# Optimization experiments

Hardware: AMD Instinct MI355X
Metric: run time of the kernel (lower is better)

The kernel has to match this reference:

```python
import jax, jax.numpy as jnp
import numpy as np

B, C, H, W = 8, 128, 128, 128
HEADS = 4
EPS_LN = 1e-6
EPS_NORM = 1e-12


def layernorm2d(x, w, b):
    # channel-wise LN over axis 1 of (B,C,H,W)
    mean = x.mean(axis=1, keepdims=True)
    var = ((x - mean) ** 2).mean(axis=1, keepdims=True)
    xn = (x - mean) / jnp.sqrt(var + EPS_LN)
    return xn * w[None, :, None, None] + b[None, :, None, None]


def conv1x1(x, w):
    # w: (O, C) pointwise conv, no bias
    return jnp.einsum('bchw,oc->bohw', x, w)


def dwconv3x3(x, w):
    # w: (C, 1, 3, 3) depthwise conv, SAME padding, no bias
    return jax.lax.conv_general_dilated(
        x, w, window_strides=(1, 1), padding='SAME',
        dimension_numbers=('NCHW', 'OIHW', 'NCHW'),
        feature_group_count=x.shape[1])


def l2norm_lastdim(x):
    n = jnp.sqrt(jnp.sum(x * x, axis=-1, keepdims=True))
    return x / jnp.maximum(n, EPS_NORM)


def setup_inputs() -> dict:
    key = jax.random.key(0)
    ks = jax.random.split(key, 12)
    s = 0.05
    return {
        'state': jax.random.normal(ks[0], (B, C, H, W), jnp.float32),
        'dark': jax.random.normal(ks[1], (B, C, H, W), jnp.float32),
        'nq_w': jnp.ones((C,), jnp.float32),
        'nq_b': jnp.zeros((C,), jnp.float32),
        'nkv_w': jnp.ones((C,), jnp.float32),
        'nkv_b': jnp.zeros((C,), jnp.float32),
        'q_pw': jax.random.normal(ks[2], (C, C), jnp.float32) * s,
        'q_dw': jax.random.normal(ks[3], (C, 1, 3, 3), jnp.float32) * s,
        'k_pw': jax.random.normal(ks[4], (C, C), jnp.float32) * s,
        'k_dw': jax.random.normal(ks[5], (C, 1, 3, 3), jnp.float32) * s,
        'v_pw': jax.random.normal(ks[6], (C, C), jnp.float32) * s,
        'v_dw': jax.random.normal(ks[7], (C, 1, 3, 3), jnp.float32) * s,
        'proj_w': jax.random.normal(ks[8], (C, C), jnp.float32) * s,
        'temperature': jnp.ones((HEADS, 1, 1), jnp.float32),
    }


def reference(state, dark, nq_w, nq_b, nkv_w, nkv_b, q_pw, q_dw, k_pw, k_dw,
              v_pw, v_dw, proj_w, temperature):
    b, c, h, w = state.shape
    dc = c // HEADS
    residual = state

    q = dwconv3x3(conv1x1(layernorm2d(state, nq_w, nq_b), q_pw), q_dw)
    k = dwconv3x3(conv1x1(layernorm2d(dark, nkv_w, nkv_b), k_pw), k_dw)
    v = dwconv3x3(conv1x1(dark, v_pw), v_dw)

    q = q.reshape(b, HEADS, dc, h * w)
    k = k.reshape(b, HEADS, dc, h * w)
    v = v.reshape(b, HEADS, dc, h * w)

    q = l2norm_lastdim(q)
    k = l2norm_lastdim(k)

    # channel-wise attention map: (b, heads, dc, dc)
    attn = jnp.einsum('bhcd,bhed->bhce', q, k) * temperature[None]
    attn = jax.nn.softmax(attn, axis=-1)

    out = jnp.einsum('bhce,bhed->bhcd', attn, v).reshape(b, c, h, w)
    return conv1x1(out, proj_w) + residual
```

## Files before the change

kernel.cpp:

```cpp
#include <hip/hip_runtime.h>
#include <hip/hip_bf16.h>
#include <cstdint>

#define BB 8
#define CC 128
#define HH 128
#define WWID 128
#define HW (HH * WWID)
#define NHEADS 4
#define DC (CC / NHEADS)

typedef unsigned short u16x8 __attribute__((ext_vector_type(8)));
typedef unsigned short u16x4 __attribute__((ext_vector_type(4)));
typedef short s16x8 __attribute__((ext_vector_type(8)));
typedef float f32x4 __attribute__((ext_vector_type(4)));

__device__ __forceinline__ float bf2f(unsigned short u) {
  union { unsigned int i; float f; } c;
  c.i = ((unsigned int)u) << 16;
  return c.f;
}
__device__ __forceinline__ unsigned short f2bf(float f) {
  __hip_bfloat16 h = __float2bfloat16(f);
  return *reinterpret_cast<unsigned short*>(&h);
}

__device__ __forceinline__ void quad_transpose(float& v0, float& v1, float& v2,
                                               float& v3, int r) {
  float u0 = __shfl_xor(v0, 1), u1 = __shfl_xor(v1, 1);
  float u2 = __shfl_xor(v2, 1), u3 = __shfl_xor(v3, 1);
  if ((r & 1) == 0) { v1 = u0; v3 = u2; } else { v0 = u1; v2 = u3; }
  u0 = __shfl_xor(v0, 2); u1 = __shfl_xor(v1, 2);
  u2 = __shfl_xor(v2, 2); u3 = __shfl_xor(v3, 2);
  if ((r & 2) == 0) { v2 = u0; v3 = u1; } else { v0 = u2; v1 = u3; }
}

__global__ __launch_bounds__(128) void prep_weights_kernel(
    const float* __restrict__ q_pw, const float* __restrict__ k_pw,
    const float* __restrict__ v_pw, const float* __restrict__ proj_w,
    const float* __restrict__ nq_w, const float* __restrict__ nq_b,
    const float* __restrict__ nkv_w, const float* __restrict__ nkv_b,
    unsigned short* __restrict__ Wq, unsigned short* __restrict__ Wkv,
    unsigned short* __restrict__ Wproj, float* __restrict__ S1q,
    float* __restrict__ S2q, float* __restrict__ S1k, float* __restrict__ S2k) {
  int o = threadIdx.x;
  int which = blockIdx.x;
  if (which == 0) {
    float s1 = 0.f, s2 = 0.f;
    for (int c = 0; c < CC; ++c) {
      float w = q_pw[o * CC + c];
      float wl = w * nq_w[c];
      s1 += wl;
      s2 += w * nq_b[c];
      Wq[o * CC + c] = f2bf(wl);
    }
    S1q[o] = s1;
    S2q[o] = s2;
  } else if (which == 1) {
    float s1 = 0.f, s2 = 0.f;
    for (int c = 0; c < CC; ++c) {
      float w = k_pw[o * CC + c];
      float wl = w * nkv_w[c];
      s1 += wl;
      s2 += w * nkv_b[c];
      Wkv[o * CC + c] = f2bf(wl);
    }
    S1k[o] = s1;
    S2k[o] = s2;
  } else if (which == 2) {
    for (int c = 0; c < CC; ++c) Wkv[(128 + o) * CC + c] = f2bf(v_pw[o * CC + c]);
  } else {
    for (int c = 0; c < CC; ++c) Wproj[o * CC + c] = f2bf(proj_w[o * CC + c]);
  }
}

template <int MT, int LN_ROWS, int IN_BF16, int OUT_F32, int DO_RES>
__global__ __launch_bounds__(256) void conv_mfma_kernel(
    const void* __restrict__ Xv, const unsigned short* __restrict__ Wbf,
    const float* __restrict__ S1, const float* __restrict__ S2,
    const float* __restrict__ res, unsigned short* __restrict__ Out0,
    unsigned short* __restrict__ Out1, float* __restrict__ OutF) {
  constexpr int MPW = MT / 4;
  __shared__ unsigned short Xs[64 * 128];
  __shared__ float sstat[2][4][64];
  __shared__ float muA[64], rrA[64];

  int tid = threadIdx.x;
  int lane = tid & 63, wid = tid >> 6;
  int b = blockIdx.y;
  int p0 = blockIdx.x * 64;

  int r = tid & 3;
  int pg = (tid >> 2) & 15;
  float s = 0.f, ss = 0.f;
  size_t xbase = (size_t)b * CC * HW + p0 + pg * 4;
#pragma unroll
  for (int i = 0; i < 8; ++i) {
    int cb = i * 16 + wid * 4;
    int ch = cb + r;
    float v0, v1, v2, v3;
    if (IN_BF16) {
      u16x4 u = *(const u16x4*)((const unsigned short*)Xv + xbase + (size_t)ch * HW);
      v0 = bf2f(u[0]); v1 = bf2f(u[1]); v2 = bf2f(u[2]); v3 = bf2f(u[3]);
    } else {
      float4 f = *(const float4*)((const float*)Xv + xbase + (size_t)ch * HW);
      v0 = f.x; v1 = f.y; v2 = f.z; v3 = f.w;
    }
    quad_transpose(v0, v1, v2, v3, r);
    if (LN_ROWS > 0) {
      s += v0 + v1 + v2 + v3;
      ss += v0 * v0 + v1 * v1 + v2 * v2 + v3 * v3;
    }
    int p = pg * 4 + r;
    u16x4 o;
    o[0] = f2bf(v0); o[1] = f2bf(v1); o[2] = f2bf(v2); o[3] = f2bf(v3);
    *(u16x4*)((char*)Xs + p * 256 + ((cb * 2) ^ ((p & 7) << 4))) = o;
  }
  if (LN_ROWS > 0) {
    int p = pg * 4 + r;
    sstat[0][wid][p] = s;
    sstat[1][wid][p] = ss;
  }
  __syncthreads();

  if (LN_ROWS > 0 && wid == 0) {
    float t1 = sstat[0][0][lane] + sstat[0][1][lane] + sstat[0][2][lane] + sstat[0][3][lane];
    float t2 = sstat[1][0][lane] + sstat[1][1][lane] + sstat[1][2][lane] + sstat[1][3][lane];
    float mu = t1 * (1.f / 128.f);
    float var = t2 * (1.f / 128.f) - mu * mu;
    muA[lane] = mu;
    rrA[lane] = rsqrtf(var + 1e-6f);
  }

  f32x4 acc[MPW][4];
#pragma unroll
  for (int mi = 0; mi < MPW; ++mi)
#pragma unroll
    for (int n = 0; n < 4; ++n) acc[mi][n] = (f32x4){0.f, 0.f, 0.f, 0.f};

#pragma unroll
  for (int kk = 0; kk < 4; ++kk) {
    s16x8 af[MPW], bfr[4];
#pragma unroll
    for (int mi = 0; mi < MPW; ++mi) {
      int o = wid * (MPW * 16) + mi * 16 + (lane & 15);
      af[mi] = *(const s16x8*)(Wbf + (size_t)o * CC + kk * 32 + (lane >> 4) * 8);
    }
#pragma unroll
    for (int n = 0; n < 4; ++n) {
      int pp = n * 16 + (lane & 15);
      int colb = (kk * 64 + (lane >> 4) * 16) ^ ((pp & 7) << 4);
      bfr[n] = *(s16x8*)((char*)Xs + pp * 256 + colb);
    }
#pragma unroll
    for (int mi = 0; mi < MPW; ++mi)
#pragma unroll
      for (int n = 0; n < 4; ++n)
        acc[mi][n] =
            __builtin_amdgcn_mfma_f32_16x16x32_bf16(af[mi], bfr[n], acc[mi][n], 0, 0, 0);
  }

  if (LN_ROWS > 0) __syncthreads();

  int q = (lane >> 2) & 3, m = lane & 3, g = lane >> 4;
#pragma unroll
  for (int mi = 0; mi < MPW; ++mi) {
    int o_base = wid * (MPW * 16) + mi * 16;
    int o = o_base + g * 4 + m;
    bool ln = (LN_ROWS > 0) && (o_base < LN_ROWS);
    float s1v = 0.f, s2v = 0.f;
    if (ln) { s1v = S1[o]; s2v = S2[o]; }
#pragma unroll
    for (int n = 0; n < 4; ++n) {
      float v0 = acc[mi][n][0], v1 = acc[mi][n][1], v2 = acc[mi][n][2], v3 = acc[mi][n][3];
      quad_transpose(v0, v1, v2, v3, m);
      int px0 = n * 16 + q * 4;
      if (ln) {
        float4 muv = *(float4*)&muA[px0];
        float4 rrv = *(float4*)&rrA[px0];
        v0 = rrv.x * (v0 - muv.x * s1v) + s2v;
        v1 = rrv.y * (v1 - muv.y * s1v) + s2v;
        v2 = rrv.z * (v2 - muv.z * s1v) + s2v;
        v3 = rrv.w * (v3 - muv.w * s1v) + s2v;
      }
      if (OUT_F32) {
        size_t off = ((size_t)b * CC + o) * HW + p0 + px0;
        if (DO_RES) {
          float4 rv = *(const float4*)(res + off);
          v0 += rv.x; v1 += rv.y; v2 += rv.z; v3 += rv.w;
        }
        float4 ov = {v0, v1, v2, v3};
        *(float4*)(OutF + off) = ov;
      } else {
        unsigned short* dst = Out0;
        int od = o;
        if (MT == 16 && o >= 128) { dst = Out1; od = o - 128; }
        u16x4 ov;
        ov[0] = f2bf(v0); ov[1] = f2bf(v1); ov[2] = f2bf(v2); ov[3] = f2bf(v3);
        *(u16x4*)(dst + ((size_t)b * CC + od) * HW + p0 + px0) = ov;
      }
    }
  }
}

template <int NORM>
__global__ __launch_bounds__(256) void dwconv_kernel(
    const unsigned short* __restrict__ X, const float* __restrict__ Wd,
    unsigned short* __restrict__ Out, float* __restrict__ normOut) {
  __shared__ float plane[34 * 128];
  int strip = blockIdx.x & 3;
  int bc = blockIdx.x >> 2;
  int c = bc & (CC - 1);
  int y0 = strip * 32;
  const unsigned short* src = X + (size_t)bc * HW;
  int tid = threadIdx.x;

  for (int idx = tid; idx < 34 * 16; idx += 256) {
    int row = idx >> 4;
    int x8 = (idx & 15) * 8;
    int y = y0 - 1 + row;
    float4 f0 = {0, 0, 0, 0}, f1 = {0, 0, 0, 0};
    if (y >= 0 && y < HH) {
      u16x8 v = *(const u16x8*)(src + (size_t)y * WWID + x8);
      f0 = make_float4(bf2f(v[0]), bf2f(v[1]), bf2f(v[2]), bf2f(v[3]));
      f1 = make_float4(bf2f(v[4]), bf2f(v[5]), bf2f(v[6]), bf2f(v[7]));
    }
    *(float4*)&plane[row * 128 + x8] = f0;
    *(float4*)&plane[row * 128 + x8 + 4] = f1;
  }
  float w[9];
#pragma unroll
  for (int j = 0; j < 9; ++j) w[j] = Wd[c * 9 + j];
  __syncthreads();

  float ssq = 0.f;
  unsigned short* dst = Out + (size_t)bc * HW + y0 * WWID;
#pragma unroll
  for (int i = 0; i < 4; ++i) {
    int pix4 = i * 1024 + tid * 4;
    int ly = pix4 >> 7, x0 = pix4 & 127;
    const float* pc = &plane[(ly + 1) * 128 + x0];
    float sv[4];
    if (x0 >= 4 && x0 <= 120) {
#pragma unroll
      for (int dx = 0; dx < 4; ++dx)
        sv[dx] = w[0] * pc[dx - 129] + w[1] * pc[dx - 128] + w[2] * pc[dx - 127] +
                 w[3] * pc[dx - 1] + w[4] * pc[dx] + w[5] * pc[dx + 1] +
                 w[6] * pc[dx + 127] + w[7] * pc[dx + 128] + w[8] * pc[dx + 129];
    } else {
#pragma unroll
      for (int dx = 0; dx < 4; ++dx) {
        int x = x0 + dx;
        float a = 0.f;
        for (int dy = -1; dy <= 1; ++dy)
          for (int dx2 = -1; dx2 <= 1; ++dx2) {
            int xx = x + dx2;
            if (xx >= 0 && xx < WWID)
              a += w[(dy + 1) * 3 + dx2 + 1] * plane[(ly + 1 + dy) * 128 + xx];
          }
        sv[dx] = a;
      }
    }
    if (NORM) ssq += sv[0] * sv[0] + sv[1] * sv[1] + sv[2] * sv[2] + sv[3] * sv[3];
    u16x4 o;
#pragma unroll
    for (int dx = 0; dx < 4; ++dx) o[dx] = f2bf(sv[dx]);
    *(u16x4*)(dst + pix4) = o;
  }
  if (NORM) {
#pragma unroll
    for (int m2 = 32; m2 >= 1; m2 >>= 1) ssq += __shfl_xor(ssq, m2, 64);
    __shared__ float sred[4];
    if ((tid & 63) == 0) sred[tid >> 6] = ssq;
    __syncthreads();
    if (tid == 0) atomicAdd(&normOut[bc], sred[0] + sred[1] + sred[2] + sred[3]);
  }
}

__global__ __launch_bounds__(256) void qk_partial_kernel(
    const unsigned short* __restrict__ Q, const unsigned short* __restrict__ K,
    float* __restrict__ part) {
  __shared__ float qs[32][129];
  __shared__ float ks[32][129];
  int ksid = blockIdx.x;
  int bh = blockIdx.y;
  int b = bh >> 2, h = bh & 3;
  size_t base = ((size_t)b * CC + h * DC) * HW + ksid * 512;
  int tid = threadIdx.x;
  int ci0 = (tid >> 4) * 2, ce0 = (tid & 15) * 2;
  float a00 = 0, a01 = 0, a10 = 0, a11 = 0;
  for (int ch = 0; ch < 4; ++ch) {
#pragma unroll
    for (int i = 0; i < 2; ++i) {
      int idx = i * 256 + tid;
      int rr = idx >> 4, c8 = (idx & 15) * 8;
      u16x8 qv = *(const u16x8*)(Q + base + (size_t)rr * HW + ch * 128 + c8);
      u16x8 kv = *(const u16x8*)(K + base + (size_t)rr * HW + ch * 128 + c8);
#pragma unroll
      for (int j = 0; j < 8; ++j) {
        qs[rr][c8 + j] = bf2f(qv[j]);
        ks[rr][c8 + j] = bf2f(kv[j]);
      }
    }
    __syncthreads();
    for (int p = 0; p < 128; ++p) {
      float q0 = qs[ci0][p], q1 = qs[ci0 + 1][p];
      float k0 = ks[ce0][p], k1 = ks[ce0 + 1][p];
      a00 += q0 * k0;
      a01 += q0 * k1;
      a10 += q1 * k0;
      a11 += q1 * k1;
    }
    __syncthreads();
  }
  float* o = part + ((size_t)bh * 32 + ksid) * 1024;
  o[ci0 * 32 + ce0] = a00;
  o[ci0 * 32 + ce0 + 1] = a01;
  o[(ci0 + 1) * 32 + ce0] = a10;
  o[(ci0 + 1) * 32 + ce0 + 1] = a11;
}

__global__ __launch_bounds__(1024) void softmax_kernel(
    const float* __restrict__ part, const float* __restrict__ rq,
    const float* __restrict__ rk, const float* __restrict__ temp,
    float* __restrict__ attn) {
  int bh = blockIdx.x;
  int b = bh >> 2, h = bh & 3;
  int tid = threadIdx.x;
  int c = tid >> 5, e = tid & 31;
  const float* p0 = part + (size_t)bh * 32 * 1024 + tid;
  float s = 0.f;
#pragma unroll
  for (int ks = 0; ks < 32; ++ks) s += p0[(size_t)ks * 1024];
  float nq = sqrtf(rq[b * CC + h * DC + c]);
  float nk = sqrtf(rk[b * CC + h * DC + e]);
  s *= temp[h] / (fmaxf(nq, 1e-12f) * fmaxf(nk, 1e-12f));
  float m = s;
#pragma unroll
  for (int w2 = 16; w2 >= 1; w2 >>= 1) m = fmaxf(m, __shfl_xor(m, w2, 64));
  float pe = __expf(s - m);
  float sum = pe;
#pragma unroll
  for (int w2 = 16; w2 >= 1; w2 >>= 1) sum += __shfl_xor(sum, w2, 64);
  attn[(size_t)bh * 1024 + tid] = pe / sum;
}

__global__ __launch_bounds__(256) void av_kernel(
    const float* __restrict__ attn, const unsigned short* __restrict__ V,
    unsigned short* __restrict__ Out) {
  __shared__ float vs[32][260];
  __shared__ float as[32][32];
  int pt = blockIdx.x, bh = blockIdx.y;
  int b = bh >> 2, h = bh & 3;
  size_t vbase = ((size_t)b * CC + h * DC) * HW + pt * 256;
  int tid = threadIdx.x;
#pragma unroll
  for (int i = 0; i < 4; ++i) {
    int idx = i * 256 + tid;
    int rr = idx >> 5, c8 = (idx & 31) * 8;
    u16x8 vv = *(const u16x8*)(V + vbase + (size_t)rr * HW + c8);
#pragma unroll
    for (int j = 0; j < 8; ++j) vs[rr][c8 + j] = bf2f(vv[j]);
  }
#pragma unroll
  for (int i = 0; i < 4; ++i)
    ((float*)as)[i * 256 + tid] = attn[(size_t)bh * 1024 + i * 256 + tid];
  __syncthreads();

  int cg = tid >> 6;
  int p4 = (tid & 63) * 4;
  float4 acc[8];
#pragma unroll
  for (int ci = 0; ci < 8; ++ci) acc[ci] = make_float4(0.f, 0.f, 0.f, 0.f);
  for (int e = 0; e < 32; ++e) {
    float4 v4 = *(float4*)&vs[e][p4];
#pragma unroll
    for (int ci = 0; ci < 8; ++ci) {
      float a = as[cg * 8 + ci][e];
      acc[ci].x += a * v4.x;
      acc[ci].y += a * v4.y;
      acc[ci].z += a * v4.z;
      acc[ci].w += a * v4.w;
    }
  }
#pragma unroll
  for (int ci = 0; ci < 8; ++ci) {
    size_t off = ((size_t)b * CC + h * DC + cg * 8 + ci) * HW + pt * 256 + p4;
    u16x4 o;
    o[0] = f2bf(acc[ci].x);
    o[1] = f2bf(acc[ci].y);
    o[2] = f2bf(acc[ci].z);
    o[3] = f2bf(acc[ci].w);
    *(u16x4*)(Out + off) = o;
  }
}

extern "C" void kernel_launch(void* const* d_in, const int* in_sizes, int n_in,
                              void* d_out, int out_size, void* d_ws, size_t ws_size,
                              hipStream_t stream) {
  (void)in_sizes; (void)n_in; (void)out_size; (void)ws_size;
  const float* state = (const float*)d_in[0];
  const float* dark = (const float*)d_in[1];
  const float* nq_w = (const float*)d_in[2];
  const float* nq_b = (const float*)d_in[3];
  const float* nkv_w = (const float*)d_in[4];
  const float* nkv_b = (const float*)d_in[5];
  const float* q_pw = (const float*)d_in[6];
  const float* q_dw = (const float*)d_in[7];
  const float* k_pw = (const float*)d_in[8];
  const float* k_dw = (const float*)d_in[9];
  const float* v_pw = (const float*)d_in[10];
  const float* v_dw = (const float*)d_in[11];
  const float* proj_w = (const float*)d_in[12];
  const float* temp = (const float*)d_in[13];
  float* out = (float*)d_out;

  char* ws = (char*)d_ws;
  const size_t REG = 32ull << 20;
  unsigned short* R0 = (unsigned short*)(ws + 0 * REG);
  unsigned short* R1 = (unsigned short*)(ws + 1 * REG);
  unsigned short* R2 = (unsigned short*)(ws + 2 * REG);
  unsigned short* R3 = (unsigned short*)(ws + 3 * REG);
  char* sm = ws + 4 * REG;
  float* part = (float*)sm; sm += (size_t)32 * 32 * 1024 * 4;
  float* attn = (float*)sm; sm += (size_t)32 * 1024 * 4;
  float* rq = (float*)sm; sm += BB * CC * 4;
  float* rk = (float*)sm; sm += BB * CC * 4;
  unsigned short* Wq = (unsigned short*)sm; sm += (size_t)CC * CC * 2;
  unsigned short* Wkv = (unsigned short*)sm; sm += (size_t)2 * CC * CC * 2;
  unsigned short* Wproj = (unsigned short*)sm; sm += (size_t)CC * CC * 2;
  float* S1q = (float*)sm; sm += CC * 4;
  float* S2q = (float*)sm; sm += CC * 4;
  float* S1k = (float*)sm; sm += CC * 4;
  float* S2k = (float*)sm; sm += CC * 4;

  hipMemsetAsync(rq, 0, 2 * BB * CC * sizeof(float), stream);

  prep_weights_kernel<<<dim3(4), 128, 0, stream>>>(
      q_pw, k_pw, v_pw, proj_w, nq_w, nq_b, nkv_w, nkv_b, Wq, Wkv, Wproj, S1q,
      S2q, S1k, S2k);

  dim3 cgrid(HW / 64, BB);
  conv_mfma_kernel<8, 128, 0, 0, 0><<<cgrid, 256, 0, stream>>>(
      state, Wq, S1q, S2q, nullptr, R0, nullptr, nullptr);
  dwconv_kernel<1><<<dim3(BB * CC * 4), 256, 0, stream>>>(R0, q_dw, R1, rq);

  conv_mfma_kernel<16, 128, 0, 0, 0><<<cgrid, 256, 0, stream>>>(
      dark, Wkv, S1k, S2k, nullptr, R2, R3, nullptr);
  dwconv_kernel<1><<<dim3(BB * CC * 4), 256, 0, stream>>>(R2, k_dw, R0, rk);
  dwconv_kernel<0><<<dim3(BB * CC * 4), 256, 0, stream>>>(R3, v_dw, R2, nullptr);

  qk_partial_kernel<<<dim3(32, BB * NHEADS), 256, 0, stream>>>(R1, R0, part);
  softmax_kernel<<<dim3(BB * NHEADS), 1024, 0, stream>>>(part, rq, rk, temp, attn);

  av_kernel<<<dim3(HW / 256, BB * NHEADS), 256, 0, stream>>>(attn, R2, R3);

  conv_mfma_kernel<8, 0, 1, 1, 1><<<cgrid, 256, 0, stream>>>(
      R3, Wproj, nullptr, nullptr, state, nullptr, nullptr, out);
}
```

Before: 468.2 us.

## Merge QKV pointwise convs and depthwise convs into batched launches with 128-pixel tiles

The three pointwise conv launches become one conv3_kernel using a z grid dimension for q, k and v. Each block now covers 128 pixels instead of 64, and results are staged through shared memory so global stores are coalesced 16-byte writes. The three depthwise conv launches likewise become one kernel with a y dimension, and the projection gets its own 128-pixel-tile kernel. The aim is fewer launches, more parallelism per launch and better store coalescing, at the cost of more LDS per block (32KB), which may lower occupancy. The input dark is now read twice, once for k and once for v.

```diff
diff --git a/kernel.cpp b/kernel.cpp
--- a/kernel.cpp
+++ b/kernel.cpp
@@ -40,9 +40,10 @@
     const float* __restrict__ v_pw, const float* __restrict__ proj_w,
     const float* __restrict__ nq_w, const float* __restrict__ nq_b,
     const float* __restrict__ nkv_w, const float* __restrict__ nkv_b,
-    unsigned short* __restrict__ Wq, unsigned short* __restrict__ Wkv,
-    unsigned short* __restrict__ Wproj, float* __restrict__ S1q,
-    float* __restrict__ S2q, float* __restrict__ S1k, float* __restrict__ S2k) {
+    unsigned short* __restrict__ Wq, unsigned short* __restrict__ Wk,
+    unsigned short* __restrict__ Wv, unsigned short* __restrict__ Wproj,
+    float* __restrict__ S1q, float* __restrict__ S2q, float* __restrict__ S1k,
+    float* __restrict__ S2k) {
   int o = threadIdx.x;
   int which = blockIdx.x;
   if (which == 0) {
@@ -63,119 +64,117 @@
       float wl = w * nkv_w[c];
       s1 += wl;
       s2 += w * nkv_b[c];
-      Wkv[o * CC + c] = f2bf(wl);
+      Wk[o * CC + c] = f2bf(wl);
     }
     S1k[o] = s1;
     S2k[o] = s2;
   } else if (which == 2) {
-    for (int c = 0; c < CC; ++c) Wkv[(128 + o) * CC + c] = f2bf(v_pw[o * CC + c]);
+    for (int c = 0; c < CC; ++c) Wv[o * CC + c] = f2bf(v_pw[o * CC + c]);
   } else {
     for (int c = 0; c < CC; ++c) Wproj[o * CC + c] = f2bf(proj_w[o * CC + c]);
   }
 }
 
-template <int MT, int LN_ROWS, int IN_BF16, int OUT_F32, int DO_RES>
-__global__ __launch_bounds__(256) void conv_mfma_kernel(
-    const void* __restrict__ Xv, const unsigned short* __restrict__ Wbf,
-    const float* __restrict__ S1, const float* __restrict__ S2,
-    const float* __restrict__ res, unsigned short* __restrict__ Out0,
-    unsigned short* __restrict__ Out1, float* __restrict__ OutF) {
-  constexpr int MPW = MT / 4;
-  __shared__ unsigned short Xs[64 * 128];
-  __shared__ float sstat[2][4][64];
-  __shared__ float muA[64], rrA[64];
+__global__ __launch_bounds__(256) void conv3_kernel(
+    const float* __restrict__ state, const float* __restrict__ dark,
+    const unsigned short* __restrict__ Wq, const unsigned short* __restrict__ Wk,
+    const unsigned short* __restrict__ Wv, const float* __restrict__ S1q,
+    const float* __restrict__ S2q, const float* __restrict__ S1k,
+    const float* __restrict__ S2k, unsigned short* __restrict__ Cq,
+    unsigned short* __restrict__ Ck, unsigned short* __restrict__ Cv) {
+  __shared__ unsigned short Xs[128 * 128];
+  __shared__ float sstat[2][2][128];
+  __shared__ float muA[128], rrA[128];
+
+  int z = blockIdx.z;
+  const float* X = (z == 0) ? state : dark;
+  const unsigned short* W = (z == 0) ? Wq : (z == 1) ? Wk : Wv;
+  const float* S1 = (z == 0) ? S1q : S1k;
+  const float* S2 = (z == 0) ? S2q : S2k;
+  unsigned short* Out = (z == 0) ? Cq : (z == 1) ? Ck : Cv;
+  const bool do_ln = (z < 2);
 
   int tid = threadIdx.x;
   int lane = tid & 63, wid = tid >> 6;
   int b = blockIdx.y;
-  int p0 = blockIdx.x * 64;
+  int p0 = blockIdx.x * 128;
 
   int r = tid & 3;
-  int pg = (tid >> 2) & 15;
+  int qd = tid >> 2;
+  int pg = qd & 31;
+  int chalf = qd >> 5;
+  int p = pg * 4 + r;
+  size_t xbase = (size_t)b * CC * HW + p0 + pg * 4;
   float s = 0.f, ss = 0.f;
-  size_t xbase = (size_t)b * CC * HW + p0 + pg * 4;
-#pragma unroll
-  for (int i = 0; i < 8; ++i) {
-    int cb = i * 16 + wid * 4;
-    int ch = cb + r;
-    float v0, v1, v2, v3;
-    if (IN_BF16) {
-      u16x4 u = *(const u16x4*)((const unsigned short*)Xv + xbase + (size_t)ch * HW);
-      v0 = bf2f(u[0]); v1 = bf2f(u[1]); v2 = bf2f(u[2]); v3 = bf2f(u[3]);
-    } else {
-      float4 f = *(const float4*)((const float*)Xv + xbase + (size_t)ch * HW);
-      v0 = f.x; v1 = f.y; v2 = f.z; v3 = f.w;
-    }
+#pragma unroll
+  for (int i = 0; i < 16; ++i) {
+    int cb = chalf * 4 + i * 8;
+    float4 f = *(const float4*)(X + xbase + (size_t)(cb + r) * HW);
+    float v0 = f.x, v1 = f.y, v2 = f.z, v3 = f.w;
     quad_transpose(v0, v1, v2, v3, r);
-    if (LN_ROWS > 0) {
+    if (do_ln) {
       s += v0 + v1 + v2 + v3;
       ss += v0 * v0 + v1 * v1 + v2 * v2 + v3 * v3;
     }
-    int p = pg * 4 + r;
     u16x4 o;
     o[0] = f2bf(v0); o[1] = f2bf(v1); o[2] = f2bf(v2); o[3] = f2bf(v3);
     *(u16x4*)((char*)Xs + p * 256 + ((cb * 2) ^ ((p & 7) << 4))) = o;
   }
-  if (LN_ROWS > 0) {
-    int p = pg * 4 + r;
-    sstat[0][wid][p] = s;
-    sstat[1][wid][p] = ss;
+  if (do_ln) {
+    sstat[0][chalf][p] = s;
+    sstat[1][chalf][p] = ss;
   }
   __syncthreads();
 
-  if (LN_ROWS > 0 && wid == 0) {
-    float t1 = sstat[0][0][lane] + sstat[0][1][lane] + sstat[0][2][lane] + sstat[0][3][lane];
-    float t2 = sstat[1][0][lane] + sstat[1][1][lane] + sstat[1][2][lane] + sstat[1][3][lane];
-    float mu = t1 * (1.f / 128.f);
-    float var = t2 * (1.f / 128.f) - mu * mu;
-    muA[lane] = mu;
-    rrA[lane] = rsqrtf(var + 1e-6f);
-  }
-
-  f32x4 acc[MPW][4];
-#pragma unroll
-  for (int mi = 0; mi < MPW; ++mi)
-#pragma unroll
-    for (int n = 0; n < 4; ++n) acc[mi][n] = (f32x4){0.f, 0.f, 0.f, 0.f};
+  if (do_ln && wid == 0) {
+#pragma unroll
+    for (int t = 0; t < 2; ++t) {
+      int px = lane + t * 64;
+      float t1 = sstat[0][0][px] + sstat[0][1][px];
+      float t2 = sstat[1][0][px] + sstat[1][1][px];
+      float mu = t1 * (1.f / 128.f);
+      float var = t2 * (1.f / 128.f) - mu * mu;
+      muA[px] = mu;
+      rrA[px] = rsqrtf(var + 1e-6f);
+    }
+  }
+
+  f32x4 acc[2][8];
+#pragma unroll
+  for (int mi = 0; mi < 2; ++mi)
+#pragma unroll
+    for (int n = 0; n < 8; ++n) acc[mi][n] = (f32x4){0.f, 0.f, 0.f, 0.f};
 
 #pragma unroll
   for (int kk = 0; kk < 4; ++kk) {
-    s16x8 af[MPW], bfr[4];
-#pragma unroll
-    for (int mi = 0; mi < MPW; ++mi) {
-      int o = wid * (MPW * 16) + mi * 16 + (lane & 15);
-      af[mi] = *(const s16x8*)(Wbf + (size_t)o * CC + kk * 32 + (lane >> 4) * 8);
-    }
-#pragma unroll
-    for (int n = 0; n < 4; ++n) {
+    int o0 = wid * 32 + (lane & 15);
+    s16x8 af0 = *(const s16x8*)(W + (size_t)o0 * CC + kk * 32 + (lane >> 4) * 8);
+    s16x8 af1 =
+        *(const s16x8*)(W + (size_t)(o0 + 16) * CC + kk * 32 + (lane >> 4) * 8);
+#pragma unroll
+    for (int n = 0; n < 8; ++n) {
       int pp = n * 16 + (lane & 15);
       int colb = (kk * 64 + (lane >> 4) * 16) ^ ((pp & 7) << 4);
-      bfr[n] = *(s16x8*)((char*)Xs + pp * 256 + colb);
-    }
-#pragma unroll
-    for (int mi = 0; mi < MPW; ++mi)
-#pragma unroll
-      for (int n = 0; n < 4; ++n)
-        acc[mi][n] =
-            __builtin_amdgcn_mfma_f32_16x16x32_bf16(af[mi], bfr[n], acc[mi][n], 0, 0, 0);
-  }
-
-  if (LN_ROWS > 0) __syncthreads();
-
-  int q = (lane >> 2) & 3, m = lane & 3, g = lane >> 4;
-#pragma unroll
-  for (int mi = 0; mi < MPW; ++mi) {
-    int o_base = wid * (MPW * 16) + mi * 16;
-    int o = o_base + g * 4 + m;
-    bool ln = (LN_ROWS > 0) && (o_base < LN_ROWS);
+      s16x8 bv = *(s16x8*)((char*)Xs + pp * 256 + colb);
+      acc[0][n] = __builtin_amdgcn_mfma_f32_16x16x32_bf16(af0, bv, acc[0][n], 0, 0, 0);
+      acc[1][n] = __builtin_amdgcn_mfma_f32_16x16x32_bf16(af1, bv, acc[1][n], 0, 0, 0);
+    }
+  }
+  __syncthreads();
+
+  int g = lane >> 4, q = (lane >> 2) & 3, m = lane & 3;
+#pragma unroll
+  for (int mi = 0; mi < 2; ++mi) {
+    int o = wid * 32 + mi * 16 + g * 4 + m;
     float s1v = 0.f, s2v = 0.f;
-    if (ln) { s1v = S1[o]; s2v = S2[o]; }
-#pragma unroll
-    for (int n = 0; n < 4; ++n) {
-      float v0 = acc[mi][n][0], v1 = acc[mi][n][1], v2 = acc[mi][n][2], v3 = acc[mi][n][3];
+    if (do_ln) { s1v = S1[o]; s2v = S2[o]; }
+#pragma unroll
+    for (int n = 0; n < 8; ++n) {
+      float v0 = acc[mi][n][0], v1 = acc[mi][n][1], v2 = acc[mi][n][2],
+            v3 = acc[mi][n][3];
       quad_transpose(v0, v1, v2, v3, m);
       int px0 = n * 16 + q * 4;
-      if (ln) {
+      if (do_ln) {
         float4 muv = *(float4*)&muA[px0];
         float4 rrv = *(float4*)&rrA[px0];
         v0 = rrv.x * (v0 - muv.x * s1v) + s2v;
@@ -183,31 +182,104 @@
         v2 = rrv.z * (v2 - muv.z * s1v) + s2v;
         v3 = rrv.w * (v3 - muv.w * s1v) + s2v;
       }
-      if (OUT_F32) {
-        size_t off = ((size_t)b * CC + o) * HW + p0 + px0;
-        if (DO_RES) {
-          float4 rv = *(const float4*)(res + off);
-          v0 += rv.x; v1 += rv.y; v2 += rv.z; v3 += rv.w;
-        }
-        float4 ov = {v0, v1, v2, v3};
-        *(float4*)(OutF + off) = ov;
-      } else {
-        unsigned short* dst = Out0;
-        int od = o;
-        if (MT == 16 && o >= 128) { dst = Out1; od = o - 128; }
-        u16x4 ov;
-        ov[0] = f2bf(v0); ov[1] = f2bf(v1); ov[2] = f2bf(v2); ov[3] = f2bf(v3);
-        *(u16x4*)(dst + ((size_t)b * CC + od) * HW + p0 + px0) = ov;
-      }
-    }
-  }
-}
-
-template <int NORM>
-__global__ __launch_bounds__(256) void dwconv_kernel(
-    const unsigned short* __restrict__ X, const float* __restrict__ Wd,
-    unsigned short* __restrict__ Out, float* __restrict__ normOut) {
+      u16x4 ov;
+      ov[0] = f2bf(v0); ov[1] = f2bf(v1); ov[2] = f2bf(v2); ov[3] = f2bf(v3);
+      *(u16x4*)((char*)Xs + o * 256 + ((px0 * 2) ^ ((o & 7) << 4))) = ov;
+    }
+  }
+  __syncthreads();
+
+#pragma unroll
+  for (int it = 0; it < 8; ++it) {
+    int row = it * 16 + (tid >> 4);
+    int colb = ((tid & 15) * 16) ^ ((row & 7) << 4);
+    u16x8 vv = *(u16x8*)((char*)Xs + row * 256 + colb);
+    *(u16x8*)(Out + ((size_t)b * CC + row) * HW + p0 + (tid & 15) * 8) = vv;
+  }
+}
+
+__global__ __launch_bounds__(256) void proj_kernel(
+    const unsigned short* __restrict__ Xin, const unsigned short* __restrict__ Wp,
+    const float* __restrict__ res, float* __restrict__ Out) {
+  __shared__ unsigned short Xs[128 * 128];
+
+  int tid = threadIdx.x;
+  int lane = tid & 63, wid = tid >> 6;
+  int b = blockIdx.y;
+  int p0 = blockIdx.x * 128;
+
+  int r = tid & 3;
+  int qd = tid >> 2;
+  int pg = qd & 31;
+  int chalf = qd >> 5;
+  int p = pg * 4 + r;
+  size_t xbase = (size_t)b * CC * HW + p0 + pg * 4;
+#pragma unroll
+  for (int i = 0; i < 16; ++i) {
+    int cb = chalf * 4 + i * 8;
+    u16x4 u = *(const u16x4*)(Xin + xbase + (size_t)(cb + r) * HW);
+    float v0 = bf2f(u[0]), v1 = bf2f(u[1]), v2 = bf2f(u[2]), v3 = bf2f(u[3]);
+    quad_transpose(v0, v1, v2, v3, r);
+    u16x4 o;
+    o[0] = f2bf(v0); o[1] = f2bf(v1); o[2] = f2bf(v2); o[3] = f2bf(v3);
+    *(u16x4*)((char*)Xs + p * 256 + ((cb * 2) ^ ((p & 7) << 4))) = o;
+  }
+  __syncthreads();
+
+  f32x4 acc[2][8];
+#pragma unroll
+  for (int mi = 0; mi < 2; ++mi)
+#pragma unroll
+    for (int n = 0; n < 8; ++n) acc[mi][n] = (f32x4){0.f, 0.f, 0.f, 0.f};
+
+#pragma unroll
+  for (int kk = 0; kk < 4; ++kk) {
+    int o0 = wid * 32 + (lane & 15);
+    s16x8 af0 = *(const s16x8*)(Wp + (size_t)o0 * CC + kk * 32 + (lane >> 4) * 8);
+    s16x8 af1 =
+        *(const s16x8*)(Wp + (size_t)(o0 + 16) * CC + kk * 32 + (lane >> 4) * 8);
+#pragma unroll
+    for (int n = 0; n < 8; ++n) {
+      int pp = n * 16 + (lane & 15);
+      int colb = (kk * 64 + (lane >> 4) * 16) ^ ((pp & 7) << 4);
+      s16x8 bv = *(s16x8*)((char*)Xs + pp * 256 + colb);
+      acc[0][n] = __builtin_amdgcn_mfma_f32_16x16x32_bf16(af0, bv, acc[0][n], 0, 0, 0);
+      acc[1][n] = __builtin_amdgcn_mfma_f32_16x16x32_bf16(af1, bv, acc[1][n], 0, 0, 0);
+    }
+  }
+
+  int g = lane >> 4, q = (lane >> 2) & 3, m = lane & 3;
+#pragma unroll
+  for (int mi = 0; mi < 2; ++mi) {
+    int o = wid * 32 + mi * 16 + g * 4 + m;
+#pragma unroll
+    for (int n = 0; n < 8; ++n) {
+      float v0 = acc[mi][n][0], v1 = acc[mi][n][1], v2 = acc[mi][n][2],
+            v3 = acc[mi][n][3];
+      quad_transpose(v0, v1, v2, v3, m);
+      int px0 = n * 16 + q * 4;
+      size_t off = ((size_t)b * CC + o) * HW + p0 + px0;
+      float4 rv = *(const float4*)(res + off);
+      float4 ov = {v0 + rv.x, v1 + rv.y, v2 + rv.z, v3 + rv.w};
+      *(float4*)(Out + off) = ov;
+    }
+  }
+}
+
+__global__ __launch_bounds__(256) void dwconv3_kernel(
+    const unsigned short* __restrict__ Cq, const unsigned short* __restrict__ Ck,
+    const unsigned short* __restrict__ Cv, const float* __restrict__ q_dw,
+    const float* __restrict__ k_dw, const float* __restrict__ v_dw,
+    unsigned short* __restrict__ Qo, unsigned short* __restrict__ Ko,
+    unsigned short* __restrict__ Vo, float* __restrict__ rq,
+    float* __restrict__ rk) {
   __shared__ float plane[34 * 128];
+  int z = blockIdx.y;
+  const unsigned short* X = (z == 0) ? Cq : (z == 1) ? Ck : Cv;
+  const float* Wd = (z == 0) ? q_dw : (z == 1) ? k_dw : v_dw;
+  unsigned short* Out = (z == 0) ? Qo : (z == 1) ? Ko : Vo;
+  float* normOut = (z == 0) ? rq : (z == 1) ? rk : nullptr;
+
   int strip = blockIdx.x & 3;
   int bc = blockIdx.x >> 2;
   int c = bc & (CC - 1);
@@ -261,13 +333,13 @@
         sv[dx] = a;
       }
     }
-    if (NORM) ssq += sv[0] * sv[0] + sv[1] * sv[1] + sv[2] * sv[2] + sv[3] * sv[3];
+    if (normOut) ssq += sv[0] * sv[0] + sv[1] * sv[1] + sv[2] * sv[2] + sv[3] * sv[3];
     u16x4 o;
 #pragma unroll
     for (int dx = 0; dx < 4; ++dx) o[dx] = f2bf(sv[dx]);
     *(u16x4*)(dst + pix4) = o;
   }
-  if (NORM) {
+  if (normOut) {
 #pragma unroll
     for (int m2 = 32; m2 >= 1; m2 >>= 1) ssq += __shfl_xor(ssq, m2, 64);
     __shared__ float sred[4];
@@ -303,9 +375,9 @@
       }
     }
     __syncthreads();
-    for (int p = 0; p < 128; ++p) {
-      float q0 = qs[ci0][p], q1 = qs[ci0 + 1][p];
-      float k0 = ks[ce0][p], k1 = ks[ce0 + 1][p];
+    for (int pp = 0; pp < 128; ++pp) {
+      float q0 = qs[ci0][pp], q1 = qs[ci0 + 1][pp];
+      float k0 = ks[ce0][pp], k1 = ks[ce0 + 1][pp];
       a00 += q0 * k0;
       a01 += q0 * k1;
       a10 += q1 * k0;
@@ -421,13 +493,16 @@
   unsigned short* R1 = (unsigned short*)(ws + 1 * REG);
   unsigned short* R2 = (unsigned short*)(ws + 2 * REG);
   unsigned short* R3 = (unsigned short*)(ws + 3 * REG);
-  char* sm = ws + 4 * REG;
+  unsigned short* R4 = (unsigned short*)(ws + 4 * REG);
+  unsigned short* R5 = (unsigned short*)(ws + 5 * REG);
+  char* sm = ws + 6 * REG;
   float* part = (float*)sm; sm += (size_t)32 * 32 * 1024 * 4;
   float* attn = (float*)sm; sm += (size_t)32 * 1024 * 4;
   float* rq = (float*)sm; sm += BB * CC * 4;
   float* rk = (float*)sm; sm += BB * CC * 4;
   unsigned short* Wq = (unsigned short*)sm; sm += (size_t)CC * CC * 2;
-  unsigned short* Wkv = (unsigned short*)sm; sm += (size_t)2 * CC * CC * 2;
+  unsigned short* Wk = (unsigned short*)sm; sm += (size_t)CC * CC * 2;
+  unsigned short* Wv = (unsigned short*)sm; sm += (size_t)CC * CC * 2;
   unsigned short* Wproj = (unsigned short*)sm; sm += (size_t)CC * CC * 2;
   float* S1q = (float*)sm; sm += CC * 4;
   float* S2q = (float*)sm; sm += CC * 4;
@@ -437,24 +512,19 @@
   hipMemsetAsync(rq, 0, 2 * BB * CC * sizeof(float), stream);
 
   prep_weights_kernel<<<dim3(4), 128, 0, stream>>>(
-      q_pw, k_pw, v_pw, proj_w, nq_w, nq_b, nkv_w, nkv_b, Wq, Wkv, Wproj, S1q,
-      S2q, S1k, S2k);
-
-  dim3 cgrid(HW / 64, BB);
-  conv_mfma_kernel<8, 128, 0, 0, 0><<<cgrid, 256, 0, stream>>>(
-      state, Wq, S1q, S2q, nullptr, R0, nullptr, nullptr);
-  dwconv_kernel<1><<<dim3(BB * CC * 4), 256, 0, stream>>>(R0, q_dw, R1, rq);
-
-  conv_mfma_kernel<16, 128, 0, 0, 0><<<cgrid, 256, 0, stream>>>(
-      dark, Wkv, S1k, S2k, nullptr, R2, R3, nullptr);
-  dwconv_kernel<1><<<dim3(BB * CC * 4), 256, 0, stream>>>(R2, k_dw, R0, rk);
-  dwconv_kernel<0><<<dim3(BB * CC * 4), 256, 0, stream>>>(R3, v_dw, R2, nullptr);
-
-  qk_partial_kernel<<<dim3(32, BB * NHEADS), 256, 0, stream>>>(R1, R0, part);
+      q_pw, k_pw, v_pw, proj_w, nq_w, nq_b, nkv_w, nkv_b, Wq, Wk, Wv, Wproj,
+      S1q, S2q, S1k, S2k);
+
+  conv3_kernel<<<dim3(HW / 128, BB, 3), 256, 0, stream>>>(
+      state, dark, Wq, Wk, Wv, S1q, S2q, S1k, S2k, R0, R2, R3);
+
+  dwconv3_kernel<<<dim3(BB * CC * 4, 3), 256, 0, stream>>>(
+      R0, R2, R3, q_dw, k_dw, v_dw, R1, R4, R5, rq, rk);
+
+  qk_partial_kernel<<<dim3(32, BB * NHEADS), 256, 0, stream>>>(R1, R4, part);
   softmax_kernel<<<dim3(BB * NHEADS), 1024, 0, stream>>>(part, rq, rk, temp, attn);
 
-  av_kernel<<<dim3(HW / 256, BB * NHEADS), 256, 0, stream>>>(attn, R2, R3);
-
-  conv_mfma_kernel<8, 0, 1, 1, 1><<<cgrid, 256, 0, stream>>>(
-      R3, Wproj, nullptr, nullptr, state, nullptr, nullptr, out);
-}
+  av_kernel<<<dim3(HW / 256, BB * NHEADS), 256, 0, stream>>>(attn, R5, R0);
+
+  proj_kernel<<<dim3(HW / 128, BB), 256, 0, stream>>>(R0, Wproj, state, out);
+}
```

Result: faster. 458.2 us (-2.1%).
